# Kernel tuning notes

Hardware: AMD Instinct MI355X
Metric: run time of the kernel (lower is better)

## Reference

```python
import jax, jax.numpy as jnp
import numpy as np


def setup_inputs() -> dict:
    key = jax.random.key(0)
    X = jax.random.normal(key, (8192, 64, 64), dtype=jnp.float32)
    return {"X": X}


def reference(X):
    # ensure_sym: symmetrize
    S = 0.5 * (X + jnp.swapaxes(X, -1, -2))  # [B, n, n]
    # matrix exp via eigendecomposition: S = V diag(w) V^T -> exp(S) = V diag(exp(w)) V^T
    w, V = jnp.linalg.eigh(S)                # w: [B, n], V: [B, n, n]
    out = jnp.einsum('bik,bk,bjk->bij', V, jnp.exp(w), V)
    return out
```

## Files before the change

### kernel.cpp

```cpp
#include <hip/hip_runtime.h>


typedef _Float16 half4v __attribute__((ext_vector_type(4)));
typedef _Float16 half8v __attribute__((ext_vector_type(8)));
typedef float f32x4 __attribute__((ext_vector_type(4)));

constexpr int N = 64;

struct Split { _Float16 h, l; };

__device__ __forceinline__ Split split16(float v) {
    Split s;
    s.h = (_Float16)v;
    s.l = (_Float16)((v - (float)s.h) * 2048.0f);
    return s;
}

__device__ __forceinline__ int swz(int row, int colbyte) {
    return (row * 128 + colbyte) ^ ((row & 7) << 4);
}

__device__ __forceinline__ half8v frag16(const char* p, int tile, int ks, int lane) {
    const int row = tile * 16 + (lane & 15);
    const int cb = (ks * 32 + ((lane >> 4) << 3)) * 2;
    return *reinterpret_cast<const half8v*>(p + swz(row, cb));
}

__device__ __forceinline__ f32x4 mm_split(const half8v* ah, const half8v* al,
                                          const half8v* bh, const half8v* bl) {
    f32x4 c = {0.f, 0.f, 0.f, 0.f};
    c = __builtin_amdgcn_mfma_f32_16x16x32_f16(al[0], bl[0], c, 0, 0, 0);
    c = __builtin_amdgcn_mfma_f32_16x16x32_f16(al[1], bl[1], c, 0, 0, 0);
    #pragma unroll
    for (int e = 0; e < 4; ++e) c[e] *= (1.0f / 2048.0f);
    c = __builtin_amdgcn_mfma_f32_16x16x32_f16(al[0], bh[0], c, 0, 0, 0);
    c = __builtin_amdgcn_mfma_f32_16x16x32_f16(al[1], bh[1], c, 0, 0, 0);
    c = __builtin_amdgcn_mfma_f32_16x16x32_f16(ah[0], bl[0], c, 0, 0, 0);
    c = __builtin_amdgcn_mfma_f32_16x16x32_f16(ah[1], bl[1], c, 0, 0, 0);
    #pragma unroll
    for (int e = 0; e < 4; ++e) c[e] *= (1.0f / 2048.0f);
    c = __builtin_amdgcn_mfma_f32_16x16x32_f16(ah[0], bh[0], c, 0, 0, 0);
    c = __builtin_amdgcn_mfma_f32_16x16x32_f16(ah[1], bh[1], c, 0, 0, 0);
    return c;
}

__global__ __launch_bounds__(256, 3) void expm64_kernel(const float* __restrict__ X,
                                                        float* __restrict__ out) {
    __shared__ alignas(16) char lds[49152];
    char* Th = lds;
    char* Tl = lds + 8192;
    char* Ph = lds + 16384;
    char* Pl = lds + 24576;
    char* Qh = lds + 32768;
    char* Ql = lds + 40960;
    float* Xs = reinterpret_cast<float*>(lds + 16384);

    const int t = threadIdx.x;
    const int lane = t & 63;
    const int wv = t >> 6;
    const int wr = (wv >> 1) << 1;
    const int wc = (wv & 1) << 1;
    const size_t base = (size_t)blockIdx.x * (N * N);

    {
        const float4* src = reinterpret_cast<const float4*>(X + base);
        float4* dst = reinterpret_cast<float4*>(Xs);
        #pragma unroll
        for (int i = 0; i < 4; ++i) dst[t + 256 * i] = src[t + 256 * i];
    }
    __syncthreads();

    const int r0 = (t >> 4) << 2;
    const int c0 = (t & 15) << 2;

    float tv[4][4];
    #pragma unroll
    for (int i = 0; i < 4; ++i) {
        half4v h, l;
        #pragma unroll
        for (int j = 0; j < 4; ++j) {
            float v = (Xs[(r0 + i) * 64 + (c0 + j)] + Xs[(c0 + j) * 64 + (r0 + i)]) * (1.0f / 32.0f);
            tv[i][j] = v;
            Split s = split16(v);
            h[j] = s.h; l[j] = s.l;
        }
        *reinterpret_cast<half4v*>(Th + swz(r0 + i, c0 * 2)) = h;
        *reinterpret_cast<half4v*>(Tl + swz(r0 + i, c0 * 2)) = l;
    }
    __syncthreads();

    {
        const float c10 = 2.755731922398589e-07f;
        const float c11 = 2.505210838544172e-08f;
        #pragma unroll
        for (int i = 0; i < 4; ++i) {
            half4v h, l;
            #pragma unroll
            for (int j = 0; j < 4; ++j) {
                float v = c11 * tv[i][j] + ((r0 + i == c0 + j) ? c10 : 0.0f);
                Split s = split16(v);
                h[j] = s.h; l[j] = s.l;
            }
            *reinterpret_cast<half4v*>(Ph + swz(r0 + i, c0 * 2)) = h;
            *reinterpret_cast<half4v*>(Pl + swz(r0 + i, c0 * 2)) = l;
        }
    }
    __syncthreads();

    {
        half8v ah[2][2], al[2][2], bh[2][2], bl[2][2];
        #pragma unroll
        for (int a = 0; a < 2; ++a)
            #pragma unroll
            for (int ks = 0; ks < 2; ++ks) {
                ah[a][ks] = frag16(Th, wr + a, ks, lane);
                al[a][ks] = frag16(Tl, wr + a, ks, lane);
                bh[a][ks] = frag16(Th, wc + a, ks, lane);
                bl[a][ks] = frag16(Tl, wc + a, ks, lane);
            }
        #pragma unroll
        for (int a = 0; a < 2; ++a)
            #pragma unroll
            for (int b = 0; b < 2; ++b) {
                f32x4 acc = mm_split(ah[a], al[a], bh[b], bl[b]);
                const int rowp = (wc + b) * 16 + (lane & 15);
                const int colp = (wr + a) * 16 + ((lane >> 4) << 2);
                half4v h, l;
                #pragma unroll
                for (int e = 0; e < 4; ++e) {
                    Split s = split16(acc[e]);
                    h[e] = s.h; l[e] = s.l;
                }
                *reinterpret_cast<half4v*>(Qh + swz(rowp, colp * 2)) = h;
                *reinterpret_cast<half4v*>(Ql + swz(rowp, colp * 2)) = l;
            }
    }
    __syncthreads();

    {
        const float ce[5] = { 2.48015873015873e-05f, 1.388888888888889e-03f,
                              4.1666666666666664e-02f, 0.5f, 1.0f };
        const float co[5] = { 2.7557319223985893e-06f, 1.984126984126984e-04f,
                              8.333333333333333e-03f, 1.6666666666666666e-01f, 1.0f };
        half8v t2h[2][2], t2l[2][2];
        #pragma unroll
        for (int b = 0; b < 2; ++b)
            #pragma unroll
            for (int ks = 0; ks < 2; ++ks) {
                t2h[b][ks] = frag16(Qh, wc + b, ks, lane);
                t2l[b][ks] = frag16(Ql, wc + b, ks, lane);
            }
        #pragma unroll
        for (int s = 0; s < 5; ++s) {
            half8v ah[2][2], al[2][2];
            #pragma unroll
            for (int a = 0; a < 2; ++a)
                #pragma unroll
                for (int ks = 0; ks < 2; ++ks) {
                    ah[a][ks] = frag16(Ph, wr + a, ks, lane);
                    al[a][ks] = frag16(Pl, wr + a, ks, lane);
                }
            f32x4 acc[2][2];
            #pragma unroll
            for (int a = 0; a < 2; ++a)
                #pragma unroll
                for (int b = 0; b < 2; ++b)
                    acc[a][b] = mm_split(ah[a], al[a], t2h[b], t2l[b]);
            __syncthreads();
            const float fin = (s == 4) ? 0.5f : 1.0f;
            #pragma unroll
            for (int a = 0; a < 2; ++a)
                #pragma unroll
                for (int b = 0; b < 2; ++b) {
                    const int rowp = (wc + b) * 16 + (lane & 15);
                    const int colp = (wr + a) * 16 + ((lane >> 4) << 2);
                    const half4v th = *reinterpret_cast<const half4v*>(Th + swz(rowp, colp * 2));
                    const half4v tl = *reinterpret_cast<const half4v*>(Tl + swz(rowp, colp * 2));
                    half4v h, l;
                    #pragma unroll
                    for (int e = 0; e < 4; ++e) {
                        const int grow = colp + e;
                        const int gcol = rowp;
                        const float tval = (float)th[e] + (float)tl[e] * (1.0f / 2048.0f);
                        const float v = (acc[a][b][e] + co[s] * tval
                                         + ((grow == gcol) ? ce[s] : 0.0f)) * fin;
                        Split sp = split16(v);
                        h[e] = sp.h; l[e] = sp.l;
                    }
                    *reinterpret_cast<half4v*>(Ph + swz(rowp, colp * 2)) = h;
                    *reinterpret_cast<half4v*>(Pl + swz(rowp, colp * 2)) = l;
                }
            __syncthreads();
        }
    }

    #pragma unroll
    for (int s = 0; s < 4; ++s) {
        half8v ah[2][2], al[2][2], bh[2][2], bl[2][2];
        #pragma unroll
        for (int a = 0; a < 2; ++a)
            #pragma unroll
            for (int ks = 0; ks < 2; ++ks) {
                ah[a][ks] = frag16(Ph, wr + a, ks, lane);
                al[a][ks] = frag16(Pl, wr + a, ks, lane);
                bh[a][ks] = frag16(Ph, wc + a, ks, lane);
                bl[a][ks] = frag16(Pl, wc + a, ks, lane);
            }
        f32x4 acc[2][2];
        #pragma unroll
        for (int a = 0; a < 2; ++a)
            #pragma unroll
            for (int b = 0; b < 2; ++b)
                acc[a][b] = mm_split(ah[a], al[a], bh[b], bl[b]);
        __syncthreads();
        #pragma unroll
        for (int a = 0; a < 2; ++a)
            #pragma unroll
            for (int b = 0; b < 2; ++b) {
                const int rowp = (wc + b) * 16 + (lane & 15);
                const int colp = (wr + a) * 16 + ((lane >> 4) << 2);
                half4v h, l;
                #pragma unroll
                for (int e = 0; e < 4; ++e) {
                    Split sp = split16(acc[a][b][e]);
                    h[e] = sp.h; l[e] = sp.l;
                }
                *reinterpret_cast<half4v*>(Ph + swz(rowp, colp * 2)) = h;
                *reinterpret_cast<half4v*>(Pl + swz(rowp, colp * 2)) = l;
            }
        __syncthreads();
    }

    {
        const int r = t >> 2;
        const int cb0 = (t & 3) << 5;
        const half8v h0 = *reinterpret_cast<const half8v*>(Ph + swz(r, cb0));
        const half8v h1 = *reinterpret_cast<const half8v*>(Ph + swz(r, cb0 + 16));
        const half8v l0 = *reinterpret_cast<const half8v*>(Pl + swz(r, cb0));
        const half8v l1 = *reinterpret_cast<const half8v*>(Pl + swz(r, cb0 + 16));
        float4* dst = reinterpret_cast<float4*>(out + base + r * 64 + ((t & 3) << 4));
        float v[16];
        #pragma unroll
        for (int e = 0; e < 8; ++e) {
            v[e]     = ((float)h0[e] + (float)l0[e] * (1.0f / 2048.0f)) * 65536.0f;
            v[8 + e] = ((float)h1[e] + (float)l1[e] * (1.0f / 2048.0f)) * 65536.0f;
        }
        #pragma unroll
        for (int q = 0; q < 4; ++q) {
            float4 o = { v[q * 4], v[q * 4 + 1], v[q * 4 + 2], v[q * 4 + 3] };
            dst[q] = o;
        }
    }
}

extern "C" void kernel_launch(void* const* d_in, const int* in_sizes, int n_in,
                              void* d_out, int out_size, void* d_ws, size_t ws_size,
                              hipStream_t stream) {
    const float* X = (const float*)d_in[0];
    float* out = (float*)d_out;
    const int batch = in_sizes[0] / (N * N);
    expm64_kernel<<<dim3(batch), dim3(256), 0, stream>>>(X, out);
}
```

Before: 353.8 us.

## Drop low-low MFMA term, pack fp16 splits, store final squaring directly

Removes the lo*lo product from the three-way split-fp16 matmul, cutting each split product from eight MFMAs to six at a small precision cost. Replaces per-element fp16 conversion with packed cvt_pkrtz conversions, which also switches rounding to round-toward-zero. The last squaring step now writes its accumulators straight to global memory instead of round-tripping through LDS with two extra barriers. The direct stores are scalar and only partly coalesced (16 consecutive floats per row group).

```diff
diff --git a/kernel.cpp b/kernel.cpp
--- a/kernel.cpp
+++ b/kernel.cpp
@@ -1,19 +1,26 @@
 #include <hip/hip_runtime.h>
 
 
+typedef _Float16 half2v __attribute__((ext_vector_type(2)));
 typedef _Float16 half4v __attribute__((ext_vector_type(4)));
 typedef _Float16 half8v __attribute__((ext_vector_type(8)));
 typedef float f32x4 __attribute__((ext_vector_type(4)));
 
 constexpr int N = 64;
 
-struct Split { _Float16 h, l; };
-
-__device__ __forceinline__ Split split16(float v) {
-    Split s;
-    s.h = (_Float16)v;
-    s.l = (_Float16)((v - (float)s.h) * 2048.0f);
-    return s;
+__device__ __forceinline__ void split2(float v0, float v1, half2v& h, half2v& l) {
+    h = __builtin_bit_cast(half2v, __builtin_amdgcn_cvt_pkrtz(v0, v1));
+    l = __builtin_bit_cast(half2v, __builtin_amdgcn_cvt_pkrtz((v0 - (float)h[0]) * 2048.0f,
+                                                              (v1 - (float)h[1]) * 2048.0f));
+}
+
+__device__ __forceinline__ void split4(float v0, float v1, float v2, float v3,
+                                       half4v& h, half4v& l) {
+    half2v h01, l01, h23, l23;
+    split2(v0, v1, h01, l01);
+    split2(v2, v3, h23, l23);
+    h[0] = h01[0]; h[1] = h01[1]; h[2] = h23[0]; h[3] = h23[1];
+    l[0] = l01[0]; l[1] = l01[1]; l[2] = l23[0]; l[3] = l23[1];
 }
 
 __device__ __forceinline__ int swz(int row, int colbyte) {
@@ -29,10 +36,6 @@
 __device__ __forceinline__ f32x4 mm_split(const half8v* ah, const half8v* al,
                                           const half8v* bh, const half8v* bl) {
     f32x4 c = {0.f, 0.f, 0.f, 0.f};
-    c = __builtin_amdgcn_mfma_f32_16x16x32_f16(al[0], bl[0], c, 0, 0, 0);
-    c = __builtin_amdgcn_mfma_f32_16x16x32_f16(al[1], bl[1], c, 0, 0, 0);
-    #pragma unroll
-    for (int e = 0; e < 4; ++e) c[e] *= (1.0f / 2048.0f);
     c = __builtin_amdgcn_mfma_f32_16x16x32_f16(al[0], bh[0], c, 0, 0, 0);
     c = __builtin_amdgcn_mfma_f32_16x16x32_f16(al[1], bh[1], c, 0, 0, 0);
     c = __builtin_amdgcn_mfma_f32_16x16x32_f16(ah[0], bl[0], c, 0, 0, 0);
@@ -76,14 +79,11 @@
     float tv[4][4];
     #pragma unroll
     for (int i = 0; i < 4; ++i) {
+        #pragma unroll
+        for (int j = 0; j < 4; ++j)
+            tv[i][j] = (Xs[(r0 + i) * 64 + (c0 + j)] + Xs[(c0 + j) * 64 + (r0 + i)]) * (1.0f / 32.0f);
         half4v h, l;
-        #pragma unroll
-        for (int j = 0; j < 4; ++j) {
-            float v = (Xs[(r0 + i) * 64 + (c0 + j)] + Xs[(c0 + j) * 64 + (r0 + i)]) * (1.0f / 32.0f);
-            tv[i][j] = v;
-            Split s = split16(v);
-            h[j] = s.h; l[j] = s.l;
-        }
+        split4(tv[i][0], tv[i][1], tv[i][2], tv[i][3], h, l);
         *reinterpret_cast<half4v*>(Th + swz(r0 + i, c0 * 2)) = h;
         *reinterpret_cast<half4v*>(Tl + swz(r0 + i, c0 * 2)) = l;
     }
@@ -94,13 +94,12 @@
         const float c11 = 2.505210838544172e-08f;
         #pragma unroll
         for (int i = 0; i < 4; ++i) {
+            float v[4];
+            #pragma unroll
+            for (int j = 0; j < 4; ++j)
+                v[j] = c11 * tv[i][j] + ((r0 + i == c0 + j) ? c10 : 0.0f);
             half4v h, l;
-            #pragma unroll
-            for (int j = 0; j < 4; ++j) {
-                float v = c11 * tv[i][j] + ((r0 + i == c0 + j) ? c10 : 0.0f);
-                Split s = split16(v);
-                h[j] = s.h; l[j] = s.l;
-            }
+            split4(v[0], v[1], v[2], v[3], h, l);
             *reinterpret_cast<half4v*>(Ph + swz(r0 + i, c0 * 2)) = h;
             *reinterpret_cast<half4v*>(Pl + swz(r0 + i, c0 * 2)) = l;
         }
@@ -126,11 +125,7 @@
                 const int rowp = (wc + b) * 16 + (lane & 15);
                 const int colp = (wr + a) * 16 + ((lane >> 4) << 2);
                 half4v h, l;
-                #pragma unroll
-                for (int e = 0; e < 4; ++e) {
-                    Split s = split16(acc[e]);
-                    h[e] = s.h; l[e] = s.l;
-                }
+                split4(acc[0], acc[1], acc[2], acc[3], h, l);
                 *reinterpret_cast<half4v*>(Qh + swz(rowp, colp * 2)) = h;
                 *reinterpret_cast<half4v*>(Ql + swz(rowp, colp * 2)) = l;
             }
@@ -176,17 +171,17 @@
                     const int colp = (wr + a) * 16 + ((lane >> 4) << 2);
                     const half4v th = *reinterpret_cast<const half4v*>(Th + swz(rowp, colp * 2));
                     const half4v tl = *reinterpret_cast<const half4v*>(Tl + swz(rowp, colp * 2));
-                    half4v h, l;
+                    float v[4];
                     #pragma unroll
                     for (int e = 0; e < 4; ++e) {
                         const int grow = colp + e;
                         const int gcol = rowp;
                         const float tval = (float)th[e] + (float)tl[e] * (1.0f / 2048.0f);
-                        const float v = (acc[a][b][e] + co[s] * tval
-                                         + ((grow == gcol) ? ce[s] : 0.0f)) * fin;
-                        Split sp = split16(v);
-                        h[e] = sp.h; l[e] = sp.l;
+                        v[e] = (acc[a][b][e] + co[s] * tval
+                                + ((grow == gcol) ? ce[s] : 0.0f)) * fin;
                     }
+                    half4v h, l;
+                    split4(v[0], v[1], v[2], v[3], h, l);
                     *reinterpret_cast<half4v*>(Ph + swz(rowp, colp * 2)) = h;
                     *reinterpret_cast<half4v*>(Pl + swz(rowp, colp * 2)) = l;
                 }
@@ -212,43 +207,32 @@
             #pragma unroll
             for (int b = 0; b < 2; ++b)
                 acc[a][b] = mm_split(ah[a], al[a], bh[b], bl[b]);
-        __syncthreads();
-        #pragma unroll
-        for (int a = 0; a < 2; ++a)
-            #pragma unroll
-            for (int b = 0; b < 2; ++b) {
-                const int rowp = (wc + b) * 16 + (lane & 15);
-                const int colp = (wr + a) * 16 + ((lane >> 4) << 2);
-                half4v h, l;
-                #pragma unroll
-                for (int e = 0; e < 4; ++e) {
-                    Split sp = split16(acc[a][b][e]);
-                    h[e] = sp.h; l[e] = sp.l;
-                }
-                *reinterpret_cast<half4v*>(Ph + swz(rowp, colp * 2)) = h;
-                *reinterpret_cast<half4v*>(Pl + swz(rowp, colp * 2)) = l;
-            }
-        __syncthreads();
-    }
-
-    {
-        const int r = t >> 2;
-        const int cb0 = (t & 3) << 5;
-        const half8v h0 = *reinterpret_cast<const half8v*>(Ph + swz(r, cb0));
-        const half8v h1 = *reinterpret_cast<const half8v*>(Ph + swz(r, cb0 + 16));
-        const half8v l0 = *reinterpret_cast<const half8v*>(Pl + swz(r, cb0));
-        const half8v l1 = *reinterpret_cast<const half8v*>(Pl + swz(r, cb0 + 16));
-        float4* dst = reinterpret_cast<float4*>(out + base + r * 64 + ((t & 3) << 4));
-        float v[16];
-        #pragma unroll
-        for (int e = 0; e < 8; ++e) {
-            v[e]     = ((float)h0[e] + (float)l0[e] * (1.0f / 2048.0f)) * 65536.0f;
-            v[8 + e] = ((float)h1[e] + (float)l1[e] * (1.0f / 2048.0f)) * 65536.0f;
-        }
-        #pragma unroll
-        for (int q = 0; q < 4; ++q) {
-            float4 o = { v[q * 4], v[q * 4 + 1], v[q * 4 + 2], v[q * 4 + 3] };
-            dst[q] = o;
+        if (s < 3) {
+            __syncthreads();
+            #pragma unroll
+            for (int a = 0; a < 2; ++a)
+                #pragma unroll
+                for (int b = 0; b < 2; ++b) {
+                    const int rowp = (wc + b) * 16 + (lane & 15);
+                    const int colp = (wr + a) * 16 + ((lane >> 4) << 2);
+                    half4v h, l;
+                    split4(acc[a][b][0], acc[a][b][1], acc[a][b][2], acc[a][b][3], h, l);
+                    *reinterpret_cast<half4v*>(Ph + swz(rowp, colp * 2)) = h;
+                    *reinterpret_cast<half4v*>(Pl + swz(rowp, colp * 2)) = l;
+                }
+            __syncthreads();
+        } else {
+            float* o = out + base;
+            #pragma unroll
+            for (int a = 0; a < 2; ++a)
+                #pragma unroll
+                for (int b = 0; b < 2; ++b) {
+                    const int row0 = (wr + a) * 16 + ((lane >> 4) << 2);
+                    const int col  = (wc + b) * 16 + (lane & 15);
+                    #pragma unroll
+                    for (int e = 0; e < 4; ++e)
+                        o[(row0 + e) * 64 + col] = acc[a][b][e] * 65536.0f;
+                }
         }
     }
 }
```

Measured after the change: 313.2 us. 1.13x faster.
